# Optimization experiments

Measured on AMD Instinct MI355X. Metric: run time of the kernel, lower is better.

Reference implementation:

```python
import jax, jax.numpy as jnp
import numpy as np


def setup_inputs() -> dict:
    key = jax.random.key(0)
    k1, k2, k3 = jax.random.split(key, 3)
    B, R, Din, D = 4096, 4096, 1024, 1024
    x = jax.random.normal(k1, (B, Din), dtype=jnp.float32)
    refs = jax.random.normal(k2, (R, Din), dtype=jnp.float32)
    W = jax.random.normal(k3, (Din, D), dtype=jnp.float32) * (1.0 / np.sqrt(Din))
    b = jnp.zeros((D,), dtype=jnp.float32)
    return {"x": x, "refs": refs, "W": W, "b": b}


def reference(x, refs, W, b) -> jnp.ndarray:
    # feature extractor (linear stand-in for the CResNet embedding)
    vin = x @ W + b          # (B, D)
    vrefs = refs @ W + b     # (R, D)
    # compute_degradation_metric: mean_r ||vin_b - vref_r||^2
    # = ||vin||^2 + mean_r ||vref_r||^2 - 2 * vin @ mean_r(vref_r)
    # Same math as the naive broadcast-sub-square-sum-mean, GEMM-friendly form.
    sq_in = jnp.sum(vin * vin, axis=1)                 # (B,)
    mean_sq_ref = jnp.mean(jnp.sum(vrefs * vrefs, axis=1))  # scalar
    mean_ref = jnp.mean(vrefs, axis=0)                 # (D,)
    cross = vin @ mean_ref                             # (B,)
    degradation_metric = sq_in + mean_sq_ref - 2.0 * cross
    return degradation_metric
```

## Files before the change

### kernel.cpp

```cpp
#include <hip/hip_runtime.h>
#include <hip/hip_bf16.h>
#include <stdint.h>


typedef __attribute__((ext_vector_type(8))) short short8;
typedef __attribute__((ext_vector_type(4))) float f32x4;

__device__ __forceinline__ short f2bf(float f) {
  uint32_t u = __builtin_bit_cast(uint32_t, f);
  uint32_t r = (u + 0x7fffu + ((u >> 16) & 1u)) >> 16;
  return (short)r;
}
__device__ __forceinline__ float bf2f(short s) {
  uint32_t u = ((uint32_t)(uint16_t)s) << 16;
  return __builtin_bit_cast(float, u);
}

#define WS_WT 16777216u
#define WS_CP 18874368u
#define WS_CS 20971520u
#define WS_TV 20975616u
#define WS_XP 20979712u
#define WS_RR 20996096u

__global__ __launch_bounds__(256) void k_prep(
    const float* __restrict__ refs, const float* __restrict__ W,
    short* __restrict__ wt, float* __restrict__ cspart, float* __restrict__ zacc) {
  __shared__ short tile[64][68];
  const int b = blockIdx.x, t = threadIdx.x;
  if (b < 512) {
    const int rblk = b;
    const int c0 = t * 4;
    float s0 = 0.f, s1 = 0.f, s2 = 0.f, s3 = 0.f;
    for (int r = rblk * 8; r < rblk * 8 + 8; ++r) {
      float4 v = *(const float4*)&refs[(size_t)r * 1024 + c0];
      s0 += v.x; s1 += v.y; s2 += v.z; s3 += v.w;
    }
    cspart[rblk * 1024 + c0 + 0] = s0;
    cspart[rblk * 1024 + c0 + 1] = s1;
    cspart[rblk * 1024 + c0 + 2] = s2;
    cspart[rblk * 1024 + c0 + 3] = s3;
  } else if (b < 768) {
    const int tb = b - 512;
    const int tk = (tb >> 4) * 64, tn = (tb & 15) * 64;
    const int kk = t >> 4, nn4 = (t & 15) * 4;
#pragma unroll
    for (int p = 0; p < 4; ++p) {
      int k = kk + p * 16;
      float4 v = *(const float4*)&W[(size_t)(tk + k) * 1024 + tn + nn4];
      tile[nn4 + 0][k] = f2bf(v.x);
      tile[nn4 + 1][k] = f2bf(v.y);
      tile[nn4 + 2][k] = f2bf(v.z);
      tile[nn4 + 3][k] = f2bf(v.w);
    }
    __syncthreads();
    const int nn = t >> 4, kk4 = (t & 15) * 4;
#pragma unroll
    for (int p = 0; p < 4; ++p) {
      int n = nn + p * 16;
      uint32_t lo = (uint16_t)tile[n][kk4 + 0] | ((uint32_t)(uint16_t)tile[n][kk4 + 1] << 16);
      uint32_t hi = (uint16_t)tile[n][kk4 + 2] | ((uint32_t)(uint16_t)tile[n][kk4 + 3] << 16);
      *(uint2*)&wt[(size_t)(tn + n) * 1024 + tk + kk4] = make_uint2(lo, hi);
    }
  } else {
    const int i = (b - 768) * 256 + t;
    ((float4*)zacc)[i]        = make_float4(0.f, 0.f, 0.f, 0.f);
    ((float4*)zacc)[i + 1024] = make_float4(0.f, 0.f, 0.f, 0.f);
  }
}

__global__ void k_colsum(const float* __restrict__ cspart, float* __restrict__ colsum) {
  __shared__ float sh[8][32];
  const int t = threadIdx.x;
  const int c = t & 31, pg = t >> 5;
  const int k = blockIdx.x * 32 + c;
  float s = 0.f;
  for (int i = 0; i < 64; ++i) s += cspart[(size_t)(pg * 64 + i) * 1024 + k];
  sh[pg][c] = s;
  __syncthreads();
  if (t < 32) {
    float tot = 0.f;
#pragma unroll
    for (int g = 0; g < 8; ++g) tot += sh[g][t];
    colsum[blockIdx.x * 32 + t] = tot;
  }
}

__global__ void k_tvec(const short* __restrict__ Wt, const float* __restrict__ colsum,
                       const float* __restrict__ bias, float* __restrict__ tv) {
  int w = threadIdx.x >> 6, l = threadIdx.x & 63;
  int n = blockIdx.x * 4 + w;
  float s = 0.f;
  for (int k = l; k < 1024; k += 64)
    s += colsum[k] * (1.0f / 4096.0f) * bf2f(Wt[(size_t)n * 1024 + k]);
#pragma unroll
  for (int off = 32; off; off >>= 1) s += __shfl_down(s, off, 64);
  if (l == 0) tv[n] = s + bias[n];
}

__global__ __launch_bounds__(512, 4) void k_main(
    const float* __restrict__ X, const float* __restrict__ R,
    const short* __restrict__ Wt, const float* __restrict__ bias,
    const float* __restrict__ tv, float* __restrict__ xpart,
    float* __restrict__ refrow) {
  __shared__ __align__(16) short As[2][128 * 64];
  __shared__ __align__(16) short Bs[2][128 * 64];
  const int t = threadIdx.x;
  const int w = t >> 6, l = t & 63;
  const int wr = w >> 2, wc = w & 3;
  const int bx = blockIdx.x;
  const int nt = bx >> 6;
  const int mt = bx & 63;
  const bool is_x = (mt < 32);
  const float* Am = is_x ? X : R;
  const int m0 = (is_x ? mt : (mt - 32)) * 128;
  const int n0 = nt * 128;

  const int srow = t >> 3;
  const int sslot = t & 7;
  const int arow = t >> 4;
  const int acol = (t & 15) * 4;
  const int asl = (t & 15) >> 1, ah = t & 1;

  f32x4 acc[4][2] = {};
  float4 areg[4];

  auto stageB = [&](int buf, int kt) {
    const int k0 = kt * 64;
#pragma unroll
    for (int issue = 0; issue < 2; ++issue) {
      const int row = srow + issue * 64;
      const int sg = sslot ^ (row & 7);
      const short* gb = Wt + ((size_t)(n0 + row) * 1024 + k0 + sg * 8);
      char* lb = (char*)&Bs[buf][0] + issue * 8192 + w * 1024;
      __builtin_amdgcn_global_load_lds(
          (const __attribute__((address_space(1))) unsigned int*)gb,
          (__attribute__((address_space(3))) unsigned int*)lb, 16, 0, 0);
    }
  };
  auto loadA = [&](int kt) {
    const int k0 = kt * 64;
#pragma unroll
    for (int i = 0; i < 4; ++i) {
      const int r = arow + i * 32;
      areg[i] = *(const float4*)&Am[(size_t)(m0 + r) * 1024 + k0 + acol];
    }
  };
  auto writeA = [&](int buf) {
#pragma unroll
    for (int i = 0; i < 4; ++i) {
      const int r = arow + i * 32;
      uint32_t lo, hi;
      asm("v_cvt_pk_bf16_f32 %0, %1, %2" : "=v"(lo) : "v"(areg[i].x), "v"(areg[i].y));
      asm("v_cvt_pk_bf16_f32 %0, %1, %2" : "=v"(hi) : "v"(areg[i].z), "v"(areg[i].w));
      char* p = (char*)&As[buf][0] + r * 128 + (((asl ^ (r & 7)) * 16) + ah * 8);
      *(uint2*)p = make_uint2(lo, hi);
    }
  };

  stageB(0, 0);
  stageB(1, 1);
  loadA(0);
  writeA(0);
  loadA(1);

  for (int kt = 0; kt < 16; ++kt) {
    asm volatile("s_waitcnt lgkmcnt(0)" ::: "memory");
    __builtin_amdgcn_s_barrier();
    const int cur = kt & 1;
#pragma unroll
    for (int kk = 0; kk < 2; ++kk) {
      short8 af[4], bfr[2];
#pragma unroll
      for (int i = 0; i < 4; ++i) {
        const int ra = wr * 64 + i * 16 + (l & 15);
        const int s = (l >> 4) + kk * 4;
        af[i] = *(const short8*)&As[cur][ra * 64 + ((s ^ (ra & 7)) * 8)];
      }
#pragma unroll
      for (int j = 0; j < 2; ++j) {
        const int rbw = wc * 32 + j * 16 + (l & 15);
        const int s = (l >> 4) + kk * 4;
        bfr[j] = *(const short8*)&Bs[cur][rbw * 64 + ((s ^ (rbw & 7)) * 8)];
      }
      __builtin_amdgcn_s_setprio(1);
#pragma unroll
      for (int i = 0; i < 4; ++i)
#pragma unroll
        for (int j = 0; j < 2; ++j)
          acc[i][j] = __builtin_amdgcn_mfma_f32_16x16x32_bf16(af[i], bfr[j], acc[i][j], 0, 0, 0);
      __builtin_amdgcn_s_setprio(0);
    }
    __builtin_amdgcn_s_barrier();
    if (kt + 2 < 16) stageB(cur, kt + 2);
    if (kt + 1 < 16) writeA((kt + 1) & 1);
    if (kt + 2 < 16) loadA(kt + 2);
  }

  float bv[2], tvv[2];
#pragma unroll
  for (int n2 = 0; n2 < 2; ++n2) {
    const int col = n0 + wc * 32 + n2 * 16 + (l & 15);
    bv[n2] = bias[col];
    tvv[n2] = tv[col];
  }
#pragma unroll
  for (int m4 = 0; m4 < 4; ++m4) {
#pragma unroll
    for (int j = 0; j < 4; ++j) {
      float sq = 0.f, cr = 0.f;
#pragma unroll
      for (int n2 = 0; n2 < 2; ++n2) {
        const float v = acc[m4][n2][j] + bv[n2];
        sq += v * v;
        cr += v * tvv[n2];
      }
#pragma unroll
      for (int off = 1; off < 16; off <<= 1) {
        sq += __shfl_xor(sq, off, 64);
        cr += __shfl_xor(cr, off, 64);
      }
      if ((l & 15) == 0) {
        const int rm = m0 + wr * 64 + m4 * 16 + (l >> 4) * 4 + j;
        if (is_x) atomicAdd(&xpart[rm], sq - 2.0f * cr);
        else      atomicAdd(&refrow[rm], sq);
      }
    }
  }
}

__global__ void k_tail(const float* __restrict__ refrow, const float* __restrict__ xpart,
                       float* __restrict__ out) {
  __shared__ float sh[16];
  const int t = threadIdx.x;
  float s = 0.f;
  for (int i = t; i < 4096; i += 1024) s += refrow[i];
#pragma unroll
  for (int off = 32; off; off >>= 1) s += __shfl_down(s, off, 64);
  const int w = t >> 6, l = t & 63;
  if (l == 0) sh[w] = s;
  __syncthreads();
  if (t == 0) {
    float tot = 0.f;
#pragma unroll
    for (int i = 0; i < 16; ++i) tot += sh[i];
    sh[0] = tot * (1.0f / 4096.0f);
  }
  __syncthreads();
  const float ms = sh[0];
  for (int i = t; i < 4096; i += 1024) out[i] = xpart[i] + ms;
}

extern "C" void kernel_launch(void* const* d_in, const int* in_sizes, int n_in,
                              void* d_out, int out_size, void* d_ws, size_t ws_size,
                              hipStream_t stream) {
  const float* x    = (const float*)d_in[0];
  const float* refs = (const float*)d_in[1];
  const float* W    = (const float*)d_in[2];
  const float* bias = (const float*)d_in[3];
  float* out = (float*)d_out;
  char* ws = (char*)d_ws;

  short* wt     = (short*)(ws + WS_WT);
  float* cspart = (float*)(ws + WS_CP);
  float* colsum = (float*)(ws + WS_CS);
  float* tvv    = (float*)(ws + WS_TV);
  float* xpart  = (float*)(ws + WS_XP);
  float* refrow = (float*)(ws + WS_RR);

  hipLaunchKernelGGL(k_prep, dim3(772), dim3(256), 0, stream, refs, W, wt, cspart, xpart);
  hipLaunchKernelGGL(k_colsum, dim3(32), dim3(256), 0, stream, cspart, colsum);
  hipLaunchKernelGGL(k_tvec, dim3(256), dim3(256), 0, stream, wt, colsum, bias, tvv);
  hipLaunchKernelGGL(k_main, dim3(512), dim3(512), 0, stream, x, refs, wt, bias, tvv, xpart, refrow);
  hipLaunchKernelGGL(k_tail, dim3(1), dim3(1024), 0, stream, refrow, xpart, out);
}
```

Baseline: 51.80 us.

## Fold mean-reference projection into main GEMM via extra MFMA on colsum

Removes the separate k_tvec kernel, which computed the mean projected reference vector. The main GEMM kernel now computes that vector itself. It stages the column sums as bf16 in LDS and broadcasts them as an A operand to extra MFMAs that reuse the already-loaded B fragments. This saves a kernel launch and a separate pass over Wt, at the cost of about 25% more MFMA work per k-step and bf16 rounding of the column sums.

```diff
diff --git a/kernel.cpp b/kernel.cpp
--- a/kernel.cpp
+++ b/kernel.cpp
@@ -19,7 +19,6 @@
 #define WS_WT 16777216u
 #define WS_CP 18874368u
 #define WS_CS 20971520u
-#define WS_TV 20975616u
 #define WS_XP 20979712u
 #define WS_RR 20996096u
 
@@ -86,25 +85,14 @@
   }
 }
 
-__global__ void k_tvec(const short* __restrict__ Wt, const float* __restrict__ colsum,
-                       const float* __restrict__ bias, float* __restrict__ tv) {
-  int w = threadIdx.x >> 6, l = threadIdx.x & 63;
-  int n = blockIdx.x * 4 + w;
-  float s = 0.f;
-  for (int k = l; k < 1024; k += 64)
-    s += colsum[k] * (1.0f / 4096.0f) * bf2f(Wt[(size_t)n * 1024 + k]);
-#pragma unroll
-  for (int off = 32; off; off >>= 1) s += __shfl_down(s, off, 64);
-  if (l == 0) tv[n] = s + bias[n];
-}
-
 __global__ __launch_bounds__(512, 4) void k_main(
     const float* __restrict__ X, const float* __restrict__ R,
     const short* __restrict__ Wt, const float* __restrict__ bias,
-    const float* __restrict__ tv, float* __restrict__ xpart,
+    const float* __restrict__ colsum, float* __restrict__ xpart,
     float* __restrict__ refrow) {
   __shared__ __align__(16) short As[2][128 * 64];
   __shared__ __align__(16) short Bs[2][128 * 64];
+  __shared__ __align__(16) short cs_lds[1024];
   const int t = threadIdx.x;
   const int w = t >> 6, l = t & 63;
   const int wr = w >> 2, wc = w & 3;
@@ -123,6 +111,7 @@
   const int asl = (t & 15) >> 1, ah = t & 1;
 
   f32x4 acc[4][2] = {};
+  f32x4 acc_t[2] = {};
   float4 areg[4];
 
   auto stageB = [&](int buf, int kt) {
@@ -163,6 +152,16 @@
   loadA(0);
   writeA(0);
   loadA(1);
+  if (t < 128) {
+    float4 c0 = *(const float4*)&colsum[t * 8];
+    float4 c1 = *(const float4*)&colsum[t * 8 + 4];
+    uint32_t p0, p1, p2, p3;
+    asm("v_cvt_pk_bf16_f32 %0, %1, %2" : "=v"(p0) : "v"(c0.x), "v"(c0.y));
+    asm("v_cvt_pk_bf16_f32 %0, %1, %2" : "=v"(p1) : "v"(c0.z), "v"(c0.w));
+    asm("v_cvt_pk_bf16_f32 %0, %1, %2" : "=v"(p2) : "v"(c1.x), "v"(c1.y));
+    asm("v_cvt_pk_bf16_f32 %0, %1, %2" : "=v"(p3) : "v"(c1.z), "v"(c1.w));
+    *(uint4*)&cs_lds[t * 8] = make_uint4(p0, p1, p2, p3);
+  }
 
   for (int kt = 0; kt < 16; ++kt) {
     asm volatile("s_waitcnt lgkmcnt(0)" ::: "memory");
@@ -170,7 +169,8 @@
     const int cur = kt & 1;
 #pragma unroll
     for (int kk = 0; kk < 2; ++kk) {
-      short8 af[4], bfr[2];
+      short8 af[4], bfr[2], csf;
+      csf = *(const short8*)&cs_lds[kt * 64 + kk * 32 + (l >> 4) * 8];
 #pragma unroll
       for (int i = 0; i < 4; ++i) {
         const int ra = wr * 64 + i * 16 + (l & 15);
@@ -189,6 +189,9 @@
 #pragma unroll
         for (int j = 0; j < 2; ++j)
           acc[i][j] = __builtin_amdgcn_mfma_f32_16x16x32_bf16(af[i], bfr[j], acc[i][j], 0, 0, 0);
+#pragma unroll
+      for (int j = 0; j < 2; ++j)
+        acc_t[j] = __builtin_amdgcn_mfma_f32_16x16x32_bf16(csf, bfr[j], acc_t[j], 0, 0, 0);
       __builtin_amdgcn_s_setprio(0);
     }
     __builtin_amdgcn_s_barrier();
@@ -202,7 +205,7 @@
   for (int n2 = 0; n2 < 2; ++n2) {
     const int col = n0 + wc * 32 + n2 * 16 + (l & 15);
     bv[n2] = bias[col];
-    tvv[n2] = tv[col];
+    tvv[n2] = acc_t[n2][0] * (1.0f / 4096.0f) + bv[n2];
   }
 #pragma unroll
   for (int m4 = 0; m4 < 4; ++m4) {
@@ -264,13 +267,11 @@
   short* wt     = (short*)(ws + WS_WT);
   float* cspart = (float*)(ws + WS_CP);
   float* colsum = (float*)(ws + WS_CS);
-  float* tvv    = (float*)(ws + WS_TV);
   float* xpart  = (float*)(ws + WS_XP);
   float* refrow = (float*)(ws + WS_RR);
 
   hipLaunchKernelGGL(k_prep, dim3(772), dim3(256), 0, stream, refs, W, wt, cspart, xpart);
   hipLaunchKernelGGL(k_colsum, dim3(32), dim3(256), 0, stream, cspart, colsum);
-  hipLaunchKernelGGL(k_tvec, dim3(256), dim3(256), 0, stream, wt, colsum, bias, tvv);
-  hipLaunchKernelGGL(k_main, dim3(512), dim3(512), 0, stream, x, refs, wt, bias, tvv, xpart, refrow);
+  hipLaunchKernelGGL(k_main, dim3(512), dim3(512), 0, stream, x, refs, wt, bias, colsum, xpart, refrow);
   hipLaunchKernelGGL(k_tail, dim3(1), dim3(1024), 0, stream, refrow, xpart, out);
 }
```

Result: faster. 46.13 us (-10.9%).
